# Performance work log

Hardware: AMD Instinct MI355X
Metric: run time of the kernel (lower is better)

The kernel has to match this reference:

```python
import jax, jax.numpy as jnp
import numpy as np

# model geometry (matches init_kwargs cfg)
D = 768        # D_EMB
PATCH = 16
T = 8192
N = T // PATCH # 512 patch tokens
H = 12         # heads
HD = D // H    # 64 head dim
NL = 6         # layers
DFF = 4 * D
B = 8
LN_EPS = 1e-5


def setup_inputs() -> dict:
    key = jax.random.key(0)
    ks = iter(jax.random.split(key, 32))
    def g(shape, scale=0.02):
        return jax.random.normal(next(ks), shape, jnp.float32) * scale
    return dict(
        x=jax.random.normal(next(ks), (B, T), jnp.float32),
        pp_w=g((D, PATCH)), pp_b=jnp.zeros((D,), jnp.float32),
        pe=g((N, D)),
        ln1_g=jnp.ones((NL, D), jnp.float32), ln1_b=jnp.zeros((NL, D), jnp.float32),
        qkv_w=g((NL, 3 * D, D)), out_w=g((NL, D, D)),
        ln2_g=jnp.ones((NL, D), jnp.float32), ln2_b=jnp.zeros((NL, D), jnp.float32),
        fc1_w=g((NL, DFF, D)), fc2_w=g((NL, D, DFF)),
        lnf_g=jnp.ones((D,), jnp.float32), lnf_b=jnp.zeros((D,), jnp.float32),
        h1_w=g((D // 2, D)), h1_b=jnp.zeros((D // 2,), jnp.float32),
        h2_w=g((2, D // 2)), h2_b=jnp.zeros((2,), jnp.float32),
    )


def _ln(x, g, b):
    m = x.mean(-1, keepdims=True)
    v = ((x - m) ** 2).mean(-1, keepdims=True)
    return (x - m) / jnp.sqrt(v + LN_EPS) * g + b


def reference(x, pp_w, pp_b, pe, ln1_g, ln1_b, qkv_w, out_w,
              ln2_g, ln2_b, fc1_w, fc2_w, lnf_g, lnf_b,
              h1_w, h1_b, h2_w, h2_b):
    Bx = x.shape[0]
    # patch embed: [B, N, PATCH] @ W^T + b -> [B, N, D]
    z = jnp.einsum('bnp,dp->bnd', x[:, :N * PATCH].reshape(Bx, N, PATCH), pp_w) + pp_b
    z = z + pe  # positional embedding (arange indexes whole table)
    mask = jnp.tril(jnp.ones((N, N), dtype=bool))
    for i in range(NL):
        # --- attention (manual causal softmax, dropout=eval/no-op) ---
        h = _ln(z, ln1_g[i], ln1_b[i])
        qkv = jnp.einsum('bnd,ed->bne', h, qkv_w[i])            # [B,N,3D]
        qkv = qkv.reshape(Bx, N, 3, H, HD).transpose(2, 0, 3, 1, 4)
        q, k, v = qkv[0], qkv[1], qkv[2]                         # [B,H,N,HD]
        s = jnp.einsum('bhld,bhmd->bhlm', q, k) / np.sqrt(HD)
        s = jnp.where(mask, s, -jnp.inf)
        a = jax.nn.softmax(s, axis=-1)
        o = jnp.einsum('bhlm,bhmd->bhld', a, v)
        o = o.transpose(0, 2, 1, 3).reshape(Bx, N, D)
        z = z + jnp.einsum('bnd,ed->bne', o, out_w[i])
        # --- FFN (exact gelu, matching F.gelu default) ---
        h = _ln(z, ln2_g[i], ln2_b[i])
        f = jax.nn.gelu(jnp.einsum('bnd,fd->bnf', h, fc1_w[i]), approximate=False)
        z = z + jnp.einsum('bnf,df->bnd', f, fc2_w[i])
    enc = _ln(z, lnf_g, lnf_b).mean(axis=1)                      # [B, D]
    y = jax.nn.relu(enc @ h1_w.T + h1_b)
    return y @ h2_w.T + h2_b                                     # [B, 2]
```

## Files before the change

kernel.cpp:

```cpp
#include <hip/hip_runtime.h>
#include <hip/hip_bf16.h>
#include <math.h>

#define D_EMB 768
#define NPATCH 16
#define NTOK 512
#define NHEAD 12
#define HDIM 64
#define NLAYER 6
#define DFF 3072
#define BATCH 8
#define MTOK (BATCH * NTOK)

typedef __attribute__((ext_vector_type(8))) short bf16x8;
typedef __attribute__((ext_vector_type(4))) float f32x4;

__device__ __forceinline__ float bf2f(ushort s) {
    unsigned u = ((unsigned)s) << 16;
    return __builtin_bit_cast(float, u);
}
__device__ __forceinline__ ushort f2bf(float f) {
    unsigned u = __builtin_bit_cast(unsigned, f);
    unsigned r = (u + 0x7FFFu + ((u >> 16) & 1u)) >> 16;
    return (ushort)r;
}

__global__ __launch_bounds__(256)
void f2bf4_kernel(const float* __restrict__ s0, ushort* __restrict__ d0, int n0,
                  const float* __restrict__ s1, ushort* __restrict__ d1, int n1,
                  const float* __restrict__ s2, ushort* __restrict__ d2, int n2,
                  const float* __restrict__ s3, ushort* __restrict__ d3, int n3)
{
    int i = blockIdx.x * 256 + threadIdx.x;
    const float* s; ushort* d; int off;
    if (i < n0)                { s = s0; d = d0; off = i; }
    else if (i < n0 + n1)      { s = s1; d = d1; off = i - n0; }
    else if (i < n0 + n1 + n2) { s = s2; d = d2; off = i - n0 - n1; }
    else if (i < n0 + n1 + n2 + n3) { s = s3; d = d3; off = i - n0 - n1 - n2; }
    else return;
    float4 v = *(const float4*)(s + (size_t)off * 4);
    ushort4 o;
    o.x = f2bf(v.x); o.y = f2bf(v.y); o.z = f2bf(v.z); o.w = f2bf(v.w);
    *(ushort4*)(d + (size_t)off * 4) = o;
}

__global__ __launch_bounds__(256)
void patch_embed_kernel(const float* __restrict__ x, const float* __restrict__ pw,
                        const float* __restrict__ pb, const float* __restrict__ pe,
                        float* __restrict__ z)
{
    int bn = blockIdx.x;
    int b = bn >> 9, n = bn & 511;
    __shared__ float xs[NPATCH];
    int t = threadIdx.x;
    if (t < NPATCH) xs[t] = x[(size_t)b * 8192 + n * NPATCH + t];
    __syncthreads();
    for (int d = t; d < D_EMB; d += 256) {
        float acc = pb[d] + pe[(size_t)n * D_EMB + d];
        const float* w = pw + (size_t)d * NPATCH;
        #pragma unroll
        for (int p = 0; p < NPATCH; ++p) acc += xs[p] * w[p];
        z[(size_t)bn * D_EMB + d] = acc;
    }
}

__device__ __forceinline__ float block_reduce_sum_256(float v)
{
    __shared__ float lds[4];
    #pragma unroll
    for (int o = 32; o > 0; o >>= 1) v += __shfl_xor(v, o);
    int lane = threadIdx.x & 63, wid = threadIdx.x >> 6;
    __syncthreads();
    if (lane == 0) lds[wid] = v;
    __syncthreads();
    return lds[0] + lds[1] + lds[2] + lds[3];
}

__device__ __forceinline__ void store_val(float* p, float v)  { *p = v; }
__device__ __forceinline__ void store_val(ushort* p, float v) { *p = f2bf(v); }

template<typename OT>
__global__ __launch_bounds__(256)
void ln_kernel(const float* __restrict__ x, const float* __restrict__ g,
               const float* __restrict__ bta, OT* __restrict__ y)
{
    int row = blockIdx.x;
    const float* xr = x + (size_t)row * D_EMB;
    int t = threadIdx.x;
    float vals[3];
    float s = 0.f;
    #pragma unroll
    for (int i = 0; i < 3; ++i) { vals[i] = xr[t + i * 256]; s += vals[i]; }
    float mean = block_reduce_sum_256(s) * (1.0f / D_EMB);
    float ss = 0.f;
    #pragma unroll
    for (int i = 0; i < 3; ++i) { float d = vals[i] - mean; ss += d * d; }
    float var = block_reduce_sum_256(ss) * (1.0f / D_EMB);
    float rstd = rsqrtf(var + 1e-5f);
    #pragma unroll
    for (int i = 0; i < 3; ++i) {
        int d = t + i * 256;
        store_val(y + (size_t)row * D_EMB + d, (vals[i] - mean) * rstd * g[d] + bta[d]);
    }
}

template<typename OT>
__global__ __launch_bounds__(256)
void reduce_ln_kernel(const float* __restrict__ pbuf, float* __restrict__ z,
                      const float* __restrict__ g, const float* __restrict__ bta,
                      OT* __restrict__ y)
{
    int row = blockIdx.x;
    int t = threadIdx.x;
    const float* p0 = pbuf + (size_t)row * D_EMB;
    const float* p1 = pbuf + (size_t)MTOK * D_EMB + (size_t)row * D_EMB;
    float* zr = z + (size_t)row * D_EMB;
    float vals[3];
    float s = 0.f;
    #pragma unroll
    for (int i = 0; i < 3; ++i) {
        int d = t + i * 256;
        float v = zr[d] + p0[d] + p1[d];
        vals[i] = v;
        zr[d] = v;
        s += v;
    }
    float mean = block_reduce_sum_256(s) * (1.0f / D_EMB);
    float ss = 0.f;
    #pragma unroll
    for (int i = 0; i < 3; ++i) { float d = vals[i] - mean; ss += d * d; }
    float var = block_reduce_sum_256(ss) * (1.0f / D_EMB);
    float rstd = rsqrtf(var + 1e-5f);
    #pragma unroll
    for (int i = 0; i < 3; ++i) {
        int d = t + i * 256;
        store_val(y + (size_t)row * D_EMB + d, (vals[i] - mean) * rstd * g[d] + bta[d]);
    }
}

#define STAGE64(buf, k0)                                                           \
    {                                                                              \
        _Pragma("unroll")                                                          \
        for (int j = 0; j < 2; ++j) {                                              \
            int row = j * 32 + srow;                                               \
            int lcol = pcol ^ (row & 7);                                           \
            const ushort* sa = Ab + (size_t)(bm + row) * lda + (k0) + (lcol << 3); \
            __builtin_amdgcn_global_load_lds(                                      \
                (const __attribute__((address_space(1))) unsigned int*)sa,         \
                (__attribute__((address_space(3))) unsigned int*)&As[buf][row * 64 + (pcol << 3)], \
                16, 0, 0);                                                         \
        }                                                                          \
        _Pragma("unroll")                                                          \
        for (int j = 0; j < 4; ++j) {                                              \
            int row = j * 32 + srow;                                               \
            int lcol = pcol ^ (row & 7);                                           \
            const ushort* sb = Wb + (size_t)(bn + row) * lda + (k0) + (lcol << 3); \
            __builtin_amdgcn_global_load_lds(                                      \
                (const __attribute__((address_space(1))) unsigned int*)sb,         \
                (__attribute__((address_space(3))) unsigned int*)&Bs[buf][row * 64 + (pcol << 3)], \
                16, 0, 0);                                                         \
        }                                                                          \
    }

#define COMPUTE64(buf)                                                             \
    {                                                                              \
        _Pragma("unroll")                                                          \
        for (int kk = 0; kk < 2; ++kk) {                                           \
            int c = kk * 4 + lg;                                                   \
            bf16x8 a[4], b[2];                                                     \
            _Pragma("unroll")                                                      \
            for (int m = 0; m < 4; ++m) {                                          \
                int row = m * 16 + lr;                                             \
                a[m] = *(const bf16x8*)(&As[buf][row * 64 + ((c ^ (row & 7)) << 3)]); \
            }                                                                      \
            _Pragma("unroll")                                                      \
            for (int n = 0; n < 2; ++n) {                                          \
                int row = w * 32 + n * 16 + lr;                                    \
                b[n] = *(const bf16x8*)(&Bs[buf][row * 64 + ((c ^ (row & 7)) << 3)]); \
            }                                                                      \
            _Pragma("unroll")                                                      \
            for (int m = 0; m < 4; ++m) {                                          \
                _Pragma("unroll")                                                  \
                for (int n = 0; n < 2; ++n)                                        \
                    acc[m][n] = __builtin_amdgcn_mfma_f32_16x16x32_bf16(a[m], b[n], acc[m][n], 0, 0, 0); \
            }                                                                      \
        }                                                                          \
    }

template<int EPI, typename OT, bool SPLITK>
__global__ __launch_bounds__(256)
void mfma_gemm(const ushort* __restrict__ A, const ushort* __restrict__ W,
               OT* __restrict__ C, const float* __restrict__ res,
               int N, int K, int lda)
{
    __shared__ ushort As[3][64 * 64];
    __shared__ ushort Bs[3][128 * 64];

    int gx = gridDim.x, gy = gridDim.y;
    int bx = blockIdx.x, by = blockIdx.y;
    int bz = SPLITK ? blockIdx.z : 0;
    if ((gy & 7) == 0) {
        int flat = bx + gx * (by + gy * bz);
        int xcd = flat & 7, j = flat >> 3;
        int ry = gy >> 3;
        by = xcd * ry + (j % ry);
        int rem = j / ry;
        bx = rem % gx;
        bz = rem / gx;
    }
    int bm = by * 64, bn = bx * 128;

    const ushort* Ab = A + (size_t)bz * K;
    const ushort* Wb = W + (size_t)bz * K;
    OT* Cb = C + (SPLITK ? (size_t)bz * ((size_t)gy * 64) * N : 0);

    int tid = threadIdx.x;
    int w = tid >> 6, l = tid & 63;
    int lr = l & 15, lg = l >> 4;
    f32x4 acc[4][2] = {};

    int srow = w * 8 + (l >> 3);
    int pcol = l & 7;

    const int nk = K >> 6;
    STAGE64(0, 0);
    STAGE64(1, 64);
    for (int t = 0; t < nk; ++t) {
        if (t < nk - 1) { asm volatile("s_waitcnt vmcnt(6)" ::: "memory"); }
        else            { asm volatile("s_waitcnt vmcnt(0)" ::: "memory"); }
        __builtin_amdgcn_s_barrier();
        if (t + 2 < nk) {
            int nb = (t + 2) % 3;
            STAGE64(nb, (t + 2) << 6);
        }
        COMPUTE64(t % 3);
    }

    int r0 = lg * 4;
    #pragma unroll
    for (int m = 0; m < 4; ++m) {
        #pragma unroll
        for (int n = 0; n < 2; ++n) {
            #pragma unroll
            for (int j = 0; j < 4; ++j) {
                int gm = bm + m * 16 + r0 + j;
                int gn = bn + w * 32 + n * 16 + lr;
                float v = acc[m][n][j];
                if (EPI == 1) v = 0.5f * v * (1.0f + erff(v * 0.70710678118654752f));
                if (EPI == 2) v += res[(size_t)gm * N + gn];
                store_val(Cb + (size_t)gm * N + gn, v);
            }
        }
    }
}

__global__ __launch_bounds__(256)
void attn_mfma_kernel(const ushort* __restrict__ qkv, ushort* __restrict__ o)
{
    int w = threadIdx.x >> 6, l = threadIdx.x & 63;
    int qt = blockIdx.x * 4 + w;
    int h = blockIdx.y, b = blockIdx.z;
    int q0 = qt * 16;
    int lr = l & 15, lg = l >> 4;

    const size_t rs = 3 * D_EMB;
    const ushort* qbase = qkv + ((size_t)(b * NTOK)) * rs + h * HDIM;
    const ushort* kbase = qbase + D_EMB;
    const ushort* vbase = qbase + 2 * D_EMB;

    bf16x8 qf[2];
    qf[0] = *(const bf16x8*)(qbase + (size_t)(q0 + lr) * rs + lg * 8);
    qf[1] = *(const bf16x8*)(qbase + (size_t)(q0 + lr) * rs + 32 + lg * 8);

    f32x4 oacc[4] = {};
    float m_j[4], l_j[4];
    #pragma unroll
    for (int j = 0; j < 4; ++j) { m_j[j] = -1e30f; l_j[j] = 0.f; }

    __shared__ ushort V_lds[4][32 * 64];
    __shared__ ushort P_lds[4][16][40];

    int ntiles = q0 / 32 + 1;
    for (int mt = 0; mt < ntiles; ++mt) {
        int m0 = mt * 32;
        #pragma unroll
        for (int is = 0; is < 4; ++is) {
            int row = is * 8 + (l >> 3);
            int colel = ((l & 7) * 8) ^ (is * 16);
            const ushort* sv = vbase + (size_t)(m0 + row) * rs + colel;
            __builtin_amdgcn_global_load_lds(
                (const __attribute__((address_space(1))) unsigned int*)sv,
                (__attribute__((address_space(3))) unsigned int*)&V_lds[w][is * 512 + l * 8],
                16, 0, 0);
        }
        f32x4 s[2] = {};
        #pragma unroll
        for (int kb = 0; kb < 2; ++kb) {
            const ushort* kr = kbase + (size_t)(m0 + kb * 16 + lr) * rs;
            bf16x8 k0 = *(const bf16x8*)(kr + lg * 8);
            bf16x8 k1 = *(const bf16x8*)(kr + 32 + lg * 8);
            s[kb] = __builtin_amdgcn_mfma_f32_16x16x32_bf16(qf[0], k0, s[kb], 0, 0, 0);
            s[kb] = __builtin_amdgcn_mfma_f32_16x16x32_bf16(qf[1], k1, s[kb], 0, 0, 0);
        }
        bool partial = (m0 + 31 > q0);
        float p[2][4], mx[4];
        #pragma unroll
        for (int j = 0; j < 4; ++j) {
            int qr = q0 + lg * 4 + j;
            float s0 = s[0][j] * 0.125f;
            float s1 = s[1][j] * 0.125f;
            if (partial) {
                if (m0 + lr > qr)      s0 = -1e30f;
                if (m0 + 16 + lr > qr) s1 = -1e30f;
            }
            p[0][j] = s0; p[1][j] = s1;
            float mm = fmaxf(s0, s1);
            mm = fmaxf(mm, __shfl_xor(mm, 1));
            mm = fmaxf(mm, __shfl_xor(mm, 2));
            mm = fmaxf(mm, __shfl_xor(mm, 4));
            mm = fmaxf(mm, __shfl_xor(mm, 8));
            mx[j] = mm;
        }
        #pragma unroll
        for (int j = 0; j < 4; ++j) {
            float mnew = fmaxf(m_j[j], mx[j]);
            float scale = __expf(m_j[j] - mnew);
            float p0 = __expf(p[0][j] - mnew);
            float p1 = __expf(p[1][j] - mnew);
            p[0][j] = p0; p[1][j] = p1;
            float rsum = p0 + p1;
            rsum += __shfl_xor(rsum, 1);
            rsum += __shfl_xor(rsum, 2);
            rsum += __shfl_xor(rsum, 4);
            rsum += __shfl_xor(rsum, 8);
            l_j[j] = l_j[j] * scale + rsum;
            m_j[j] = mnew;
            #pragma unroll
            for (int i = 0; i < 4; ++i) oacc[i][j] *= scale;
        }
        #pragma unroll
        for (int kb = 0; kb < 2; ++kb)
            #pragma unroll
            for (int j = 0; j < 4; ++j)
                P_lds[w][lg * 4 + j][kb * 16 + lr] = f2bf(p[kb][j]);
        asm volatile("s_waitcnt lgkmcnt(0)" ::: "memory");
        bf16x8 pa = *(const bf16x8*)(&P_lds[w][lr][lg * 8]);
        asm volatile("s_waitcnt vmcnt(0)" ::: "memory");
        #pragma unroll
        for (int i = 0; i < 4; ++i) {
            bf16x8 vf;
            #pragma unroll
            for (int j = 0; j < 8; ++j)
                vf[j] = (short)V_lds[w][(lg * 8 + j) * 64 + ((i * 16 + lr) ^ (lg * 16))];
            oacc[i] = __builtin_amdgcn_mfma_f32_16x16x32_bf16(pa, vf, oacc[i], 0, 0, 0);
        }
    }
    #pragma unroll
    for (int i = 0; i < 4; ++i) {
        #pragma unroll
        for (int j = 0; j < 4; ++j) {
            int qr = q0 + lg * 4 + j;
            int d  = i * 16 + lr;
            float v = oacc[i][j] / l_j[j];
            o[((size_t)(b * NTOK + qr)) * D_EMB + h * HDIM + d] = f2bf(v);
        }
    }
}

__global__ void mean_kernel(const float* __restrict__ x, float* __restrict__ enc)
{
    int b = blockIdx.x; int d = threadIdx.x;
    float s = 0.f;
    for (int n = 0; n < NTOK; ++n) s += x[((size_t)(b * NTOK + n)) * D_EMB + d];
    enc[b * D_EMB + d] = s * (1.0f / NTOK);
}

__global__ void head1_kernel(const float* __restrict__ enc, const float* __restrict__ w,
                             const float* __restrict__ bias, float* __restrict__ r)
{
    int b = blockIdx.x; int j = threadIdx.x;
    float acc = bias[j];
    const float* e = enc + b * D_EMB;
    const float* wr = w + (size_t)j * D_EMB;
    for (int k = 0; k < D_EMB; ++k) acc += e[k] * wr[k];
    r[b * 384 + j] = fmaxf(acc, 0.f);
}

__global__ void head2_kernel(const float* __restrict__ r, const float* __restrict__ w,
                             const float* __restrict__ bias, float* __restrict__ out)
{
    int idx = threadIdx.x;
    if (idx >= 16) return;
    int b = idx >> 1, j = idx & 1;
    float acc = bias[j];
    for (int k = 0; k < 384; ++k) acc += r[b * 384 + k] * w[j * 384 + k];
    out[b * 2 + j] = acc;
}

extern "C" void kernel_launch(void* const* d_in, const int* in_sizes, int n_in,
                              void* d_out, int out_size, void* d_ws, size_t ws_size,
                              hipStream_t stream)
{
    const float* x     = (const float*)d_in[0];
    const float* pp_w  = (const float*)d_in[1];
    const float* pp_b  = (const float*)d_in[2];
    const float* pe    = (const float*)d_in[3];
    const float* ln1_g = (const float*)d_in[4];
    const float* ln1_b = (const float*)d_in[5];
    const float* qkv_w = (const float*)d_in[6];
    const float* out_w = (const float*)d_in[7];
    const float* ln2_g = (const float*)d_in[8];
    const float* ln2_b = (const float*)d_in[9];
    const float* fc1_w = (const float*)d_in[10];
    const float* fc2_w = (const float*)d_in[11];
    const float* lnf_g = (const float*)d_in[12];
    const float* lnf_b = (const float*)d_in[13];
    const float* h1_w  = (const float*)d_in[14];
    const float* h1_b  = (const float*)d_in[15];
    const float* h2_w  = (const float*)d_in[16];
    const float* h2_b  = (const float*)d_in[17];
    float* out = (float*)d_out;

    char* p = (char*)d_ws;
    float*  z      = (float*)p;  p += (size_t)MTOK * D_EMB * 4;
    ushort* big_bf = (ushort*)p; p += (size_t)MTOK * DFF * 2;
    ushort* h_bf   = (ushort*)p; p += (size_t)MTOK * D_EMB * 2;
    ushort* wq_bf  = (ushort*)p; p += (size_t)3 * D_EMB * D_EMB * 2;
    ushort* wo_bf  = (ushort*)p; p += (size_t)D_EMB * D_EMB * 2;
    ushort* wf1_bf = (ushort*)p; p += (size_t)DFF * D_EMB * 2;
    ushort* wf2_bf = (ushort*)p; p += (size_t)D_EMB * DFF * 2;
    float*  pbuf   = (float*)p;  p += (size_t)2 * MTOK * D_EMB * 4;
    float*  enc    = (float*)p;  p += BATCH * D_EMB * 4;
    float*  r1     = (float*)p;  p += BATCH * 384 * 4;
    float*  lnf_out = (float*)big_bf;

    patch_embed_kernel<<<MTOK, 256, 0, stream>>>(x, pp_w, pp_b, pe, z);

    const int nq = 3 * D_EMB * D_EMB, no = D_EMB * D_EMB, nf = DFF * D_EMB;
    const int n4q = nq / 4, n4o = no / 4, n4f = nf / 4;
    const int cvt_blocks = (n4q + n4o + 2 * n4f + 255) / 256;

    ln_kernel<ushort><<<MTOK, 256, 0, stream>>>(z, ln1_g, ln1_b, h_bf);

    for (int i = 0; i < NLAYER; ++i) {
        f2bf4_kernel<<<cvt_blocks, 256, 0, stream>>>(
            qkv_w + (size_t)i * nq, wq_bf,  n4q,
            out_w + (size_t)i * no, wo_bf,  n4o,
            fc1_w + (size_t)i * nf, wf1_bf, n4f,
            fc2_w + (size_t)i * nf, wf2_bf, n4f);

        dim3 gq((3 * D_EMB) / 128, MTOK / 64);
        mfma_gemm<0, ushort, false><<<gq, 256, 0, stream>>>(h_bf, wq_bf, big_bf, nullptr,
                                                            3 * D_EMB, D_EMB, D_EMB);

        dim3 ga(NTOK / 64, NHEAD, BATCH);
        attn_mfma_kernel<<<ga, 256, 0, stream>>>(big_bf, h_bf);

        dim3 gp(D_EMB / 128, MTOK / 64);
        mfma_gemm<2, float, false><<<gp, 256, 0, stream>>>(h_bf, wo_bf, z, z,
                                                           D_EMB, D_EMB, D_EMB);

        ln_kernel<ushort><<<MTOK, 256, 0, stream>>>(z, ln2_g + i * D_EMB, ln2_b + i * D_EMB, h_bf);

        dim3 g1(DFF / 128, MTOK / 64);
        mfma_gemm<1, ushort, false><<<g1, 256, 0, stream>>>(h_bf, wf1_bf, big_bf, nullptr,
                                                            DFF, D_EMB, D_EMB);

        dim3 g2(D_EMB / 128, MTOK / 64, 2);
        mfma_gemm<0, float, true><<<g2, 256, 0, stream>>>(big_bf, wf2_bf, pbuf, nullptr,
                                                          D_EMB, DFF / 2, DFF);

        if (i < NLAYER - 1) {
            reduce_ln_kernel<ushort><<<MTOK, 256, 0, stream>>>(
                pbuf, z, ln1_g + (i + 1) * D_EMB, ln1_b + (i + 1) * D_EMB, h_bf);
        } else {
            reduce_ln_kernel<float><<<MTOK, 256, 0, stream>>>(
                pbuf, z, lnf_g, lnf_b, lnf_out);
        }
    }

    mean_kernel<<<BATCH, D_EMB, 0, stream>>>(lnf_out, enc);
    head1_kernel<<<BATCH, 384, 0, stream>>>(enc, h1_w, h1_b, r1);
    head2_kernel<<<1, 64, 0, stream>>>(r1, h2_w, h2_b, out);
}
```

Before: 1.299 ms.

## Batch weight conversion, simplify GEMM to double-buffer, load V directly in attention

Converts all layers' weights to bf16 in one launch when the workspace is large enough, instead of one conversion kernel per layer. Replaces the GEMM's triple-buffered async pipeline with explicit waits by a simpler double-buffered loop with __syncthreads. Drops the LDS staging of V in attention and gathers V elements straight from global memory with strided scalar loads. The GEMM and attention changes likely reduce latency hiding and memory coalescing, trading pipelining depth for simplicity and lower LDS use.

```diff
diff --git a/kernel.cpp b/kernel.cpp
--- a/kernel.cpp
+++ b/kernel.cpp
@@ -193,8 +193,8 @@
                OT* __restrict__ C, const float* __restrict__ res,
                int N, int K, int lda)
 {
-    __shared__ ushort As[3][64 * 64];
-    __shared__ ushort Bs[3][128 * 64];
+    __shared__ ushort As[2][64 * 64];
+    __shared__ ushort Bs[2][128 * 64];
 
     int gx = gridDim.x, gy = gridDim.y;
     int bx = blockIdx.x, by = blockIdx.y;
@@ -224,16 +224,13 @@
 
     const int nk = K >> 6;
     STAGE64(0, 0);
-    STAGE64(1, 64);
+    __syncthreads();
+    int cur = 0;
     for (int t = 0; t < nk; ++t) {
-        if (t < nk - 1) { asm volatile("s_waitcnt vmcnt(6)" ::: "memory"); }
-        else            { asm volatile("s_waitcnt vmcnt(0)" ::: "memory"); }
-        __builtin_amdgcn_s_barrier();
-        if (t + 2 < nk) {
-            int nb = (t + 2) % 3;
-            STAGE64(nb, (t + 2) << 6);
-        }
-        COMPUTE64(t % 3);
+        if (t + 1 < nk) STAGE64(cur ^ 1, (t + 1) << 6);
+        COMPUTE64(cur);
+        __syncthreads();
+        cur ^= 1;
     }
 
     int r0 = lg * 4;
@@ -277,22 +274,11 @@
     #pragma unroll
     for (int j = 0; j < 4; ++j) { m_j[j] = -1e30f; l_j[j] = 0.f; }
 
-    __shared__ ushort V_lds[4][32 * 64];
     __shared__ ushort P_lds[4][16][40];
 
     int ntiles = q0 / 32 + 1;
     for (int mt = 0; mt < ntiles; ++mt) {
         int m0 = mt * 32;
-        #pragma unroll
-        for (int is = 0; is < 4; ++is) {
-            int row = is * 8 + (l >> 3);
-            int colel = ((l & 7) * 8) ^ (is * 16);
-            const ushort* sv = vbase + (size_t)(m0 + row) * rs + colel;
-            __builtin_amdgcn_global_load_lds(
-                (const __attribute__((address_space(1))) unsigned int*)sv,
-                (__attribute__((address_space(3))) unsigned int*)&V_lds[w][is * 512 + l * 8],
-                16, 0, 0);
-        }
         f32x4 s[2] = {};
         #pragma unroll
         for (int kb = 0; kb < 2; ++kb) {
@@ -345,13 +331,12 @@
                 P_lds[w][lg * 4 + j][kb * 16 + lr] = f2bf(p[kb][j]);
         asm volatile("s_waitcnt lgkmcnt(0)" ::: "memory");
         bf16x8 pa = *(const bf16x8*)(&P_lds[w][lr][lg * 8]);
-        asm volatile("s_waitcnt vmcnt(0)" ::: "memory");
         #pragma unroll
         for (int i = 0; i < 4; ++i) {
             bf16x8 vf;
+            const ushort* vp = vbase + (size_t)(m0 + lg * 8) * rs + i * 16 + lr;
             #pragma unroll
-            for (int j = 0; j < 8; ++j)
-                vf[j] = (short)V_lds[w][(lg * 8 + j) * 64 + ((i * 16 + lr) ^ (lg * 16))];
+            for (int j = 0; j < 8; ++j) vf[j] = (short)vp[(size_t)j * rs];
             oacc[i] = __builtin_amdgcn_mfma_f32_16x16x32_bf16(pa, vf, oacc[i], 0, 0, 0);
         }
     }
@@ -421,53 +406,72 @@
     const float* h2_b  = (const float*)d_in[17];
     float* out = (float*)d_out;
 
+    const int nq = 3 * D_EMB * D_EMB, no = D_EMB * D_EMB, nf = DFF * D_EMB;
+    const size_t per_layer_w = ((size_t)nq + no + 2 * nf) * 2;
+
     char* p = (char*)d_ws;
     float*  z      = (float*)p;  p += (size_t)MTOK * D_EMB * 4;
     ushort* big_bf = (ushort*)p; p += (size_t)MTOK * DFF * 2;
     ushort* h_bf   = (ushort*)p; p += (size_t)MTOK * D_EMB * 2;
-    ushort* wq_bf  = (ushort*)p; p += (size_t)3 * D_EMB * D_EMB * 2;
-    ushort* wo_bf  = (ushort*)p; p += (size_t)D_EMB * D_EMB * 2;
-    ushort* wf1_bf = (ushort*)p; p += (size_t)DFF * D_EMB * 2;
-    ushort* wf2_bf = (ushort*)p; p += (size_t)D_EMB * DFF * 2;
     float*  pbuf   = (float*)p;  p += (size_t)2 * MTOK * D_EMB * 4;
     float*  enc    = (float*)p;  p += BATCH * D_EMB * 4;
     float*  r1     = (float*)p;  p += BATCH * 384 * 4;
+    size_t base_used = (size_t)(p - (char*)d_ws);
+    bool full = (ws_size >= base_used + NLAYER * per_layer_w);
+    int nlw = full ? NLAYER : 1;
+    ushort* wq_bf  = (ushort*)p; p += (size_t)nlw * nq * 2;
+    ushort* wo_bf  = (ushort*)p; p += (size_t)nlw * no * 2;
+    ushort* wf1_bf = (ushort*)p; p += (size_t)nlw * nf * 2;
+    ushort* wf2_bf = (ushort*)p; p += (size_t)nlw * nf * 2;
     float*  lnf_out = (float*)big_bf;
 
     patch_embed_kernel<<<MTOK, 256, 0, stream>>>(x, pp_w, pp_b, pe, z);
 
-    const int nq = 3 * D_EMB * D_EMB, no = D_EMB * D_EMB, nf = DFF * D_EMB;
-    const int n4q = nq / 4, n4o = no / 4, n4f = nf / 4;
-    const int cvt_blocks = (n4q + n4o + 2 * n4f + 255) / 256;
+    if (full) {
+        long long tq = (long long)NLAYER * nq / 4, to = (long long)NLAYER * no / 4;
+        long long tf = (long long)NLAYER * nf / 4;
+        long long tot = tq + to + 2 * tf;
+        f2bf4_kernel<<<(int)((tot + 255) / 256), 256, 0, stream>>>(
+            qkv_w, wq_bf, (int)tq, out_w, wo_bf, (int)to,
+            fc1_w, wf1_bf, (int)tf, fc2_w, wf2_bf, (int)tf);
+    }
 
     ln_kernel<ushort><<<MTOK, 256, 0, stream>>>(z, ln1_g, ln1_b, h_bf);
 
+    const int cvt_blocks = (nq / 4 + no / 4 + 2 * (nf / 4) + 255) / 256;
+
     for (int i = 0; i < NLAYER; ++i) {
-        f2bf4_kernel<<<cvt_blocks, 256, 0, stream>>>(
-            qkv_w + (size_t)i * nq, wq_bf,  n4q,
-            out_w + (size_t)i * no, wo_bf,  n4o,
-            fc1_w + (size_t)i * nf, wf1_bf, n4f,
-            fc2_w + (size_t)i * nf, wf2_bf, n4f);
+        const ushort* wq  = wq_bf  + (full ? (size_t)i * nq : 0);
+        const ushort* wo  = wo_bf  + (full ? (size_t)i * no : 0);
+        const ushort* wf1 = wf1_bf + (full ? (size_t)i * nf : 0);
+        const ushort* wf2 = wf2_bf + (full ? (size_t)i * nf : 0);
+        if (!full) {
+            f2bf4_kernel<<<cvt_blocks, 256, 0, stream>>>(
+                qkv_w + (size_t)i * nq, wq_bf,  nq / 4,
+                out_w + (size_t)i * no, wo_bf,  no / 4,
+                fc1_w + (size_t)i * nf, wf1_bf, nf / 4,
+                fc2_w + (size_t)i * nf, wf2_bf, nf / 4);
+        }
 
         dim3 gq((3 * D_EMB) / 128, MTOK / 64);
-        mfma_gemm<0, ushort, false><<<gq, 256, 0, stream>>>(h_bf, wq_bf, big_bf, nullptr,
+        mfma_gemm<0, ushort, false><<<gq, 256, 0, stream>>>(h_bf, wq, big_bf, nullptr,
                                                             3 * D_EMB, D_EMB, D_EMB);
 
         dim3 ga(NTOK / 64, NHEAD, BATCH);
         attn_mfma_kernel<<<ga, 256, 0, stream>>>(big_bf, h_bf);
 
         dim3 gp(D_EMB / 128, MTOK / 64);
-        mfma_gemm<2, float, false><<<gp, 256, 0, stream>>>(h_bf, wo_bf, z, z,
+        mfma_gemm<2, float, false><<<gp, 256, 0, stream>>>(h_bf, wo, z, z,
                                                            D_EMB, D_EMB, D_EMB);
 
         ln_kernel<ushort><<<MTOK, 256, 0, stream>>>(z, ln2_g + i * D_EMB, ln2_b + i * D_EMB, h_bf);
 
         dim3 g1(DFF / 128, MTOK / 64);
-        mfma_gemm<1, ushort, false><<<g1, 256, 0, stream>>>(h_bf, wf1_bf, big_bf, nullptr,
+        mfma_gemm<1, ushort, false><<<g1, 256, 0, stream>>>(h_bf, wf1, big_bf, nullptr,
                                                             DFF, D_EMB, D_EMB);
 
         dim3 g2(D_EMB / 128, MTOK / 64, 2);
-        mfma_gemm<0, float, true><<<g2, 256, 0, stream>>>(big_bf, wf2_bf, pbuf, nullptr,
+        mfma_gemm<0, float, true><<<g2, 256, 0, stream>>>(big_bf, wf2, pbuf, nullptr,
                                                           D_EMB, DFF / 2, DFF);
 
         if (i < NLAYER - 1) {
```

Result: faster. 1.102 ms (-15.2%).
